# Optimization experiments

Hardware: AMD Instinct MI355X
Metric: run time of the kernel (lower is better)

Reference implementation:

```python
import jax, jax.numpy as jnp
import numpy as np

N_NODES = 100000
N_HE = 50000
N_INC = 600000
D_IN = 256
D_H = 128
N_CLASSES = 40
N_LAYERS = 2


def setup_inputs() -> dict:
    key = jax.random.key(0)
    ks = jax.random.split(key, 8)
    s = lambda d: float(1.0 / np.sqrt(d))
    return {
        "x_0": jax.random.normal(ks[0], (N_NODES, D_IN), jnp.float32),
        "x_1": jax.random.normal(ks[1], (N_HE, D_IN), jnp.float32),
        "node_idx": jax.random.randint(ks[2], (N_INC,), 0, N_NODES),
        "he_idx": jax.random.randint(ks[3], (N_INC,), 0, N_HE),
        "inc_vals": jnp.ones((N_INC,), jnp.float32),
        "W_enc": jax.random.uniform(ks[4], (D_IN, D_H), jnp.float32, -s(D_IN), s(D_IN)),
        "b_enc": jnp.zeros((D_H,), jnp.float32),
        "W_msg0": jax.random.uniform(ks[5], (N_LAYERS, D_H, D_H), jnp.float32, -s(D_H), s(D_H)),
        "b_msg0": jnp.zeros((N_LAYERS, D_H), jnp.float32),
        "W_msg1": jax.random.uniform(ks[6], (N_LAYERS, 2 * D_H, D_H), jnp.float32, -s(2 * D_H), s(2 * D_H)),
        "b_msg1": jnp.zeros((N_LAYERS, D_H), jnp.float32),
        "W_out": jax.random.uniform(ks[7], (D_H, N_CLASSES), jnp.float32, -s(D_H), s(D_H)),
        "b_out": jnp.zeros((N_CLASSES,), jnp.float32),
    }


def reference(x_0, x_1, node_idx, he_idx, inc_vals, W_enc, b_enc,
              W_msg0, b_msg0, W_msg1, b_msg1, W_out, b_out):
    # Encode node/hyperedge features to hidden dim (shared to_hidden_linear).
    x0 = x_0 @ W_enc + b_enc  # (N_NODES, D_H)
    x1 = x_1 @ W_enc + b_enc  # (N_HE, D_H)
    for l in range(N_LAYERS):
        # Node -> hyperedge messaging: m0 = sigmoid(W x0)
        m0 = jax.nn.sigmoid(x0 @ W_msg0[l] + b_msg0[l])  # (N_NODES, D_H)
        # Gather node messages along incidence nnz, weight by incidence values,
        # scatter-sum into hyperedges.
        m0_he = jax.ops.segment_sum(inc_vals[:, None] * m0[node_idx], he_idx,
                                    num_segments=N_HE)  # (N_HE, D_H)
        # Hyperedge -> node messaging: m1 = sigmoid(W [x1 || m0_he])
        m1 = jax.nn.sigmoid(jnp.concatenate([x1, m0_he], axis=-1) @ W_msg1[l] + b_msg1[l])
        m1_node = jax.ops.segment_sum(inc_vals[:, None] * m1[he_idx], node_idx,
                                      num_segments=N_NODES)  # (N_NODES, D_H)
        # Default updating func: sigmoid(x + m) (dropout identity in eval mode).
        x0 = jax.nn.sigmoid(x0 + m1_node)
        x1 = jax.nn.sigmoid(x1 + m0_he)
    return x0 @ W_out + b_out  # (N_NODES, N_CLASSES)
```

## Files before the change

kernel.cpp:

```cpp
#include <hip/hip_runtime.h>
#include <hip/hip_bf16.h>
#include <math.h>

#define N_NODES 100000
#define N_HE    50000
#define N_INC   600000
#define D_IN    256
#define D_H     128
#define N_CLASSES 40

typedef __attribute__((ext_vector_type(8))) short short8;
typedef __attribute__((ext_vector_type(4))) float f32x4;

__device__ __forceinline__ float sigmoidf_(float x) {
    return __builtin_amdgcn_rcpf(1.0f + __expf(-x));
}

__device__ __forceinline__ short bfbits(float f) {
    __hip_bfloat16 h = __float2bfloat16(f);
    return *reinterpret_cast<short*>(&h);
}

__device__ __forceinline__ float bf_lo(unsigned u) { return __uint_as_float(u << 16); }
__device__ __forceinline__ float bf_hi(unsigned u) { return __uint_as_float(u & 0xffff0000u); }
__device__ __forceinline__ unsigned bfpack(float a, float b) {
    return (unsigned)(unsigned short)bfbits(a) | ((unsigned)(unsigned short)bfbits(b) << 16);
}

__device__ __forceinline__ void gload_lds16(const void* g, void* l) {
    __builtin_amdgcn_global_load_lds(
        (const __attribute__((address_space(1))) unsigned int*)g,
        (__attribute__((address_space(3))) unsigned int*)l, 16, 0, 0);
}

__global__ __launch_bounds__(256) void cvt_kernel(
    const float* __restrict__ in, unsigned short* __restrict__ out, int n8)
{
    const int stride = gridDim.x * 256;
    for (int i = blockIdx.x * 256 + threadIdx.x; i < n8; i += stride) {
        const float4 p = *(const float4*)(in + (size_t)i * 8);
        const float4 q = *(const float4*)(in + (size_t)i * 8 + 4);
        uint4 r;
        r.x = bfpack(p.x, p.y); r.y = bfpack(p.z, p.w);
        r.z = bfpack(q.x, q.y); r.w = bfpack(q.z, q.w);
        *(uint4*)(out + (size_t)i * 8) = r;
    }
}

template<int KT, bool SPLIT>
__global__ __launch_bounds__(256) void gemm_st(
    const __hip_bfloat16* __restrict__ A1,
    const __hip_bfloat16* __restrict__ A2,
    const __hip_bfloat16* __restrict__ Wt,
    const float* __restrict__ bias,
    __hip_bfloat16* __restrict__ C,
    int M, int act)
{
    __shared__ uint4 smemv[4096];
    char* const sA = (char*)smemv;
    char* const sB = (char*)smemv + 32768;

    const int tid = threadIdx.x;
    const int wave = tid >> 6, lane = tid & 63;
    const int quad = lane >> 4, nn = lane & 15;
    const int wr = wave >> 1, wc = wave & 1;
    const int row_base = blockIdx.x * 128;
    const int col_base = wc * 64;

    f32x4 acc[4][4] = {};

    for (int h = 0; h < KT; ++h) {
        const char* Asrc = (const char*)(SPLIT ? (h ? A2 : A1) : A1);
        const size_t astride = SPLIT ? 256 : (size_t)KT * 256;
        const size_t aoff = SPLIT ? 0 : (size_t)h * 256;
#pragma unroll
        for (int j = 0; j < 8; ++j) {
            const int sb = j * 4 + wave;
            const int s = sb * 64 + lane;
            const int row = s >> 4, c = s & 15;
            int grow = row_base + row; if (grow >= M) grow = M - 1;
            gload_lds16(Asrc + (size_t)grow * astride + aoff + ((c ^ (row & 7)) * 16),
                        sA + sb * 1024);
        }
#pragma unroll
        for (int j = 0; j < 8; ++j) {
            const int sb = j * 4 + wave;
            const int s = sb * 64 + lane;
            const int n = s >> 4, c = s & 15;
            gload_lds16((const char*)Wt + (size_t)n * (KT * 256) + (size_t)h * 256
                            + ((c ^ (n & 7)) * 16),
                        sB + sb * 1024);
        }
        __syncthreads();

#pragma unroll
        for (int ks = 0; ks < 4; ++ks) {
            short8 a[4], b[4];
#pragma unroll
            for (int rt = 0; rt < 4; ++rt) {
                const int row = wr * 64 + rt * 16 + nn;
                a[rt] = *(const short8*)(sA + row * 256 + (((ks * 4 + quad) ^ (row & 7)) * 16));
            }
#pragma unroll
            for (int ct = 0; ct < 4; ++ct) {
                const int n = col_base + ct * 16 + nn;
                b[ct] = *(const short8*)(sB + n * 256 + (((ks * 4 + quad) ^ (n & 7)) * 16));
            }
#pragma unroll
            for (int ct = 0; ct < 4; ++ct)
#pragma unroll
                for (int rt = 0; rt < 4; ++rt)
                    acc[rt][ct] = __builtin_amdgcn_mfma_f32_16x16x32_bf16(
                        a[rt], b[ct], acc[rt][ct], 0, 0, 0);
        }
        __syncthreads();
    }

    float bs[4];
#pragma unroll
    for (int ct = 0; ct < 4; ++ct) bs[ct] = bias[col_base + ct * 16 + nn];

    constexpr int KP = 136;
    unsigned short* sC = (unsigned short*)smemv;
#pragma unroll
    for (int rt = 0; rt < 4; ++rt) {
#pragma unroll
        for (int i = 0; i < 4; ++i) {
            const int R = wr * 64 + rt * 16 + quad * 4 + i;
#pragma unroll
            for (int ct = 0; ct < 4; ++ct) {
                float v = acc[rt][ct][i] + bs[ct];
                if (act) v = sigmoidf_(v);
                sC[R * KP + col_base + ct * 16 + nn] = (unsigned short)bfbits(v);
            }
        }
    }
    __syncthreads();

    {
        const int row = tid >> 1, half = tid & 1;
        const int gr = row_base + row;
        if (gr < M) {
            const unsigned short* srcp = sC + row * KP + half * 64;
            uint4* dstp = (uint4*)(C + (size_t)gr * 128 + half * 64);
#pragma unroll
            for (int j = 0; j < 8; ++j) dstp[j] = *(const uint4*)(srcp + j * 8);
        }
    }
}

__global__ __launch_bounds__(256) void out_gemm_mfma(
    const __hip_bfloat16* __restrict__ X,
    const __hip_bfloat16* __restrict__ Wt,
    const float* __restrict__ b, float* __restrict__ out, int M)
{
    constexpr int KP = 136;
    __shared__ uint4 sXv[1024];
    __shared__ __hip_bfloat16 sW[48 * KP];
    __shared__ float sB[48];
    __shared__ float sO[64 * 44];

    char* const sX = (char*)sXv;
    const int tid = threadIdx.x;
    const int wave = tid >> 6, lane = tid & 63;

#pragma unroll
    for (int j = 0; j < 4; ++j) {
        const int sb = j * 4 + wave;
        const int s = sb * 64 + lane;
        const int row = s >> 4, c = s & 15;
        int grow = blockIdx.x * 64 + row; if (grow >= M) grow = M - 1;
        gload_lds16((const char*)X + (size_t)grow * 256 + ((c ^ (row & 7)) * 16),
                    sX + sb * 1024);
    }
    for (int c = tid; c < 48 * 16; c += 256) {
        const int n = c >> 4, ko = (c & 15) * 8;
        *(uint4*)&sW[n * KP + ko] = *(const uint4*)&Wt[n * 128 + ko];
    }
    if (tid < 48) sB[tid] = (tid < 40) ? b[tid] : 0.0f;
    __syncthreads();

    const int quad = lane >> 4, nn = lane & 15;

    f32x4 acc[3] = {};
#pragma unroll
    for (int ks = 0; ks < 4; ++ks) {
        const int rowl = wave * 16 + nn;
        const short8 a = *(const short8*)(sX + rowl * 256 + (((ks * 4 + quad) ^ (rowl & 7)) * 16));
#pragma unroll
        for (int ct = 0; ct < 3; ++ct) {
            const short8 bf = *(const short8*)&sW[(ct * 16 + nn) * KP + ks * 32 + quad * 8];
            acc[ct] = __builtin_amdgcn_mfma_f32_16x16x32_bf16(a, bf, acc[ct], 0, 0, 0);
        }
    }

#pragma unroll
    for (int ct = 0; ct < 3; ++ct) {
        const int c = ct * 16 + nn;
        if (c < 40) {
#pragma unroll
            for (int i = 0; i < 4; ++i) {
                const int rl = wave * 16 + quad * 4 + i;
                sO[rl * 44 + c] = acc[ct][i] + sB[c];
            }
        }
    }
    __syncthreads();

    for (int c = tid; c < 640; c += 256) {
        const int row = c / 10, ch = c % 10;
        const int gr = blockIdx.x * 64 + row;
        if (gr < M)
            *(float4*)(out + (size_t)gr * 40 + ch * 4) =
                *(const float4*)(sO + row * 44 + ch * 4);
    }
}

__global__ __launch_bounds__(256) void wprep_kernel(
    const float* __restrict__ We, const float* __restrict__ Wm0,
    const float* __restrict__ Wm1, const float* __restrict__ Wout,
    __hip_bfloat16* __restrict__ Wt_enc, __hip_bfloat16* __restrict__ Wt_m0,
    __hip_bfloat16* __restrict__ Wt_m1, __hip_bfloat16* __restrict__ Wt_out)
{
    const int i = blockIdx.x * 256 + threadIdx.x;
    if (i < 32768) {
        const int n = i >> 8, k = i & 255;
        Wt_enc[n * 256 + k] = __float2bfloat16(We[k * 128 + n]);
    } else if (i < 65536) {
        int j = i - 32768; const int l = j >> 14; j &= 16383;
        const int n = j >> 7, k = j & 127;
        Wt_m0[l * 16384 + n * 128 + k] = __float2bfloat16(Wm0[l * 16384 + k * 128 + n]);
    } else if (i < 131072) {
        int j = i - 65536; const int l = j >> 15; j &= 32767;
        const int n = j >> 8, k = j & 255;
        Wt_m1[l * 32768 + n * 256 + k] = __float2bfloat16(Wm1[l * 32768 + k * 128 + n]);
    } else {
        const int j = i - 131072;
        const int n = j >> 7, k = j & 127;
        Wt_out[n * 128 + k] = (n < 40) ? __float2bfloat16(Wout[k * 40 + n])
                                       : __float2bfloat16(0.0f);
    }
}

__global__ __launch_bounds__(256) void zero_int_kernel(int* __restrict__ p, int n)
{
    const int i = blockIdx.x * 256 + threadIdx.x;
    if (i < n) p[i] = 0;
}

__global__ __launch_bounds__(256) void hist_kernel(
    const int* __restrict__ he_idx, const int* __restrict__ node_idx,
    int* __restrict__ he_cnt, int* __restrict__ node_cnt,
    int* __restrict__ he_rank, int* __restrict__ node_rank, int n)
{
    const int i = blockIdx.x * 256 + threadIdx.x;
    if (i < n) {
        he_rank[i] = atomicAdd(&he_cnt[he_idx[i]], 1);
        node_rank[i] = atomicAdd(&node_cnt[node_idx[i]], 1);
    }
}

__global__ __launch_bounds__(256) void scan1_kernel(
    int* __restrict__ data, int* __restrict__ bsums, int n)
{
    __shared__ int s[256];
    const int t = threadIdx.x;
    const int base = blockIdx.x * 1024 + t * 4;
    int4 v = make_int4(0, 0, 0, 0);
    if (base < n) v = *(const int4*)(data + base);
    s[t] = v.x + v.y + v.z + v.w;
    __syncthreads();
    for (int d = 1; d < 256; d <<= 1) {
        const int u = (t >= d) ? s[t - d] : 0;
        __syncthreads();
        s[t] += u;
        __syncthreads();
    }
    if (t == 255) bsums[blockIdx.x] = s[255];
    int e = t ? s[t - 1] : 0;
    if (base < n) {
        int4 o;
        o.x = e; e += v.x; o.y = e; e += v.y; o.z = e; e += v.z; o.w = e;
        *(int4*)(data + base) = o;
    }
}

__global__ __launch_bounds__(256) void scan2_kernel(int* __restrict__ bsums, int nb)
{
    __shared__ int s[256];
    const int t = threadIdx.x;
    const int v = (t < nb) ? bsums[t] : 0;
    s[t] = v;
    __syncthreads();
    for (int d = 1; d < 256; d <<= 1) {
        const int u = (t >= d) ? s[t - d] : 0;
        __syncthreads();
        s[t] += u;
        __syncthreads();
    }
    if (t < nb) bsums[t] = s[t] - v;
}

__global__ __launch_bounds__(256) void scan3_kernel(
    int* __restrict__ data, const int* __restrict__ bsums, int n)
{
    const int base = blockIdx.x * 1024 + threadIdx.x * 4;
    if (base >= n) return;
    const int adj = bsums[blockIdx.x] - ((base >= N_HE) ? N_INC : 0);
    int4 v = *(int4*)(data + base);
    v.x += adj; v.y += adj; v.z += adj; v.w += adj;
    *(int4*)(data + base) = v;
}

__global__ __launch_bounds__(256) void fill_kernel(
    const int* __restrict__ node_idx, const int* __restrict__ he_idx,
    const float* __restrict__ vals,
    const int* __restrict__ he_off, const int* __restrict__ node_off,
    const int* __restrict__ he_rank, const int* __restrict__ node_rank,
    int2* __restrict__ he_edge, int2* __restrict__ node_edge, int n)
{
    const int e = blockIdx.x * 256 + threadIdx.x;
    if (e >= n) return;
    const int hn = he_idx[e], nd = node_idx[e];
    const int vb = __float_as_int(vals[e]);
    he_edge[he_off[hn] + he_rank[e]] = make_int2(nd, vb);
    node_edge[node_off[nd] + node_rank[e]] = make_int2(hn, vb);
}

__device__ __forceinline__ void reduce_groups(
    int lane, float a0, float a1, float a2, float a3,
    float a4, float a5, float a6, float a7, float& s0, float& s1)
{
    const bool hb = (lane & 32) != 0;
    float t0 = hb ? a0 : a4;
    float t1 = hb ? a1 : a5;
    float t2 = hb ? a2 : a6;
    float t3 = hb ? a3 : a7;
    float r0 = __shfl_xor(t0, 32);
    float r1 = __shfl_xor(t1, 32);
    float r2 = __shfl_xor(t2, 32);
    float r3 = __shfl_xor(t3, 32);
    float e0 = (hb ? a4 : a0) + r0;
    float e1 = (hb ? a5 : a1) + r1;
    float e2 = (hb ? a6 : a2) + r2;
    float e3 = (hb ? a7 : a3) + r3;
    const bool lb = (lane & 16) != 0;
    float u0 = lb ? e0 : e2;
    float u1 = lb ? e1 : e3;
    float q0 = __shfl_xor(u0, 16);
    float q1 = __shfl_xor(u1, 16);
    s0 = (lb ? e2 : e0) + q0;
    s1 = (lb ? e3 : e1) + q1;
}

__global__ __launch_bounds__(256) void gather_he_kernel(
    const __hip_bfloat16* __restrict__ msrc,
    const __hip_bfloat16* __restrict__ x1cur,
    __hip_bfloat16* __restrict__ m0_he,
    __hip_bfloat16* __restrict__ x1next,
    const int* __restrict__ off, const int2* __restrict__ edges, int n_seg)
{
    const int wave = threadIdx.x >> 6;
    const int lane = threadIdx.x & 63;
    const int row = blockIdx.x * 4 + wave;
    if (row >= n_seg) return;
    const int start = off[row];
    const int end = (row + 1 < n_seg) ? off[row + 1] : N_INC;
    const int g = lane >> 4;
    const int l16 = lane & 15;
    float a0 = 0.f, a1 = 0.f, a2 = 0.f, a3 = 0.f;
    float a4 = 0.f, a5 = 0.f, a6 = 0.f, a7 = 0.f;
    const unsigned short* s16 = (const unsigned short*)msrc;
    int e = start;
    for (; e + 4 <= end; e += 4) {
        const int2 ed = edges[e + g];
        const float v = __int_as_float(ed.y);
        const uint4 u = *(const uint4*)(s16 + (size_t)ed.x * 128 + l16 * 8);
        a0 += bf_lo(u.x) * v; a1 += bf_hi(u.x) * v;
        a2 += bf_lo(u.y) * v; a3 += bf_hi(u.y) * v;
        a4 += bf_lo(u.z) * v; a5 += bf_hi(u.z) * v;
        a6 += bf_lo(u.w) * v; a7 += bf_hi(u.w) * v;
    }
    if (e < end) {
        const int ee = e + g;
        const int2 ed = (ee < end) ? edges[ee] : make_int2(0, 0);
        const float v = __int_as_float(ed.y);
        const uint4 u = *(const uint4*)(s16 + (size_t)ed.x * 128 + l16 * 8);
        a0 += bf_lo(u.x) * v; a1 += bf_hi(u.x) * v;
        a2 += bf_lo(u.y) * v; a3 += bf_hi(u.y) * v;
        a4 += bf_lo(u.z) * v; a5 += bf_hi(u.z) * v;
        a6 += bf_lo(u.w) * v; a7 += bf_hi(u.w) * v;
    }
    float s0, s1;
    reduce_groups(lane, a0, a1, a2, a3, a4, a5, a6, a7, s0, s1);
    const size_t o32 = (size_t)row * 64 + l16 * 4 + g;
    ((unsigned*)m0_he)[o32] = bfpack(s0, s1);
    const unsigned xu = ((const unsigned*)x1cur)[o32];
    ((unsigned*)x1next)[o32] =
        bfpack(sigmoidf_(bf_lo(xu) + s0), sigmoidf_(bf_hi(xu) + s1));
}

__global__ __launch_bounds__(256) void gather_node_kernel(
    const __hip_bfloat16* __restrict__ msrc,
    __hip_bfloat16* __restrict__ x0,
    const int* __restrict__ off, const int2* __restrict__ edges, int n_seg)
{
    const int wave = threadIdx.x >> 6;
    const int lane = threadIdx.x & 63;
    const int row = blockIdx.x * 4 + wave;
    if (row >= n_seg) return;
    const int start = off[row];
    const int end = (row + 1 < n_seg) ? off[row + 1] : N_INC;
    const int g = lane >> 4;
    const int l16 = lane & 15;
    float a0 = 0.f, a1 = 0.f, a2 = 0.f, a3 = 0.f;
    float a4 = 0.f, a5 = 0.f, a6 = 0.f, a7 = 0.f;
    const unsigned short* s16 = (const unsigned short*)msrc;
    int e = start;
    for (; e + 4 <= end; e += 4) {
        const int2 ed = edges[e + g];
        const float v = __int_as_float(ed.y);
        const uint4 u = *(const uint4*)(s16 + (size_t)ed.x * 128 + l16 * 8);
        a0 += bf_lo(u.x) * v; a1 += bf_hi(u.x) * v;
        a2 += bf_lo(u.y) * v; a3 += bf_hi(u.y) * v;
        a4 += bf_lo(u.z) * v; a5 += bf_hi(u.z) * v;
        a6 += bf_lo(u.w) * v; a7 += bf_hi(u.w) * v;
    }
    if (e < end) {
        const int ee = e + g;
        const int2 ed = (ee < end) ? edges[ee] : make_int2(0, 0);
        const float v = __int_as_float(ed.y);
        const uint4 u = *(const uint4*)(s16 + (size_t)ed.x * 128 + l16 * 8);
        a0 += bf_lo(u.x) * v; a1 += bf_hi(u.x) * v;
        a2 += bf_lo(u.y) * v; a3 += bf_hi(u.y) * v;
        a4 += bf_lo(u.z) * v; a5 += bf_hi(u.z) * v;
        a6 += bf_lo(u.w) * v; a7 += bf_hi(u.w) * v;
    }
    float s0, s1;
    reduce_groups(lane, a0, a1, a2, a3, a4, a5, a6, a7, s0, s1);
    const size_t o32 = (size_t)row * 64 + l16 * 4 + g;
    unsigned* px = (unsigned*)x0 + o32;
    const unsigned xu = *px;
    *px = bfpack(sigmoidf_(bf_lo(xu) + s0), sigmoidf_(bf_hi(xu) + s1));
}

extern "C" void kernel_launch(void* const* d_in, const int* in_sizes, int n_in,
                              void* d_out, int out_size, void* d_ws, size_t ws_size,
                              hipStream_t stream)
{
    const float* x0_in   = (const float*)d_in[0];
    const float* x1_in   = (const float*)d_in[1];
    const int*   node_idx = (const int*)d_in[2];
    const int*   he_idx   = (const int*)d_in[3];
    const float* inc_vals = (const float*)d_in[4];
    const float* W_enc   = (const float*)d_in[5];
    const float* b_enc   = (const float*)d_in[6];
    const float* W_msg0  = (const float*)d_in[7];
    const float* b_msg0  = (const float*)d_in[8];
    const float* W_msg1  = (const float*)d_in[9];
    const float* b_msg1  = (const float*)d_in[10];
    const float* W_out   = (const float*)d_in[11];
    const float* b_out   = (const float*)d_in[12];
    float* out = (float*)d_out;

    __hip_bfloat16* x0h    = (__hip_bfloat16*)d_ws;
    __hip_bfloat16* x1a    = x0h + 12800000;
    __hip_bfloat16* x1b    = x1a + 6400000;
    __hip_bfloat16* mbuf   = x1b + 6400000;
    __hip_bfloat16* m0_he  = mbuf + 12800000;
    __hip_bfloat16* Wt_enc = m0_he + 6400000;
    __hip_bfloat16* Wt_m0  = Wt_enc + 32768;
    __hip_bfloat16* Wt_m1  = Wt_m0 + 32768;
    __hip_bfloat16* Wt_out = Wt_m1 + 65536;
    int*  he_off    = (int*)(Wt_out + 6144);
    int*  node_off  = he_off + N_HE;
    int*  bsums     = node_off + N_NODES;
    int*  he_rank   = bsums + 256;
    int*  node_rank = he_rank + N_INC;
    int2* he_edge   = (int2*)(node_rank + N_INC);
    int2* node_edge = he_edge + N_INC;

    __hip_bfloat16* x0bf = x1b;
    __hip_bfloat16* x1bf = x1b;

    zero_int_kernel<<<(N_HE + N_NODES + 255) / 256, 256, 0, stream>>>(
        he_off, N_HE + N_NODES);
    hist_kernel<<<(N_INC + 255) / 256, 256, 0, stream>>>(
        he_idx, node_idx, he_off, node_off, he_rank, node_rank, N_INC);
    const int scan_n = N_HE + N_NODES;
    const int scan_blocks = (scan_n + 1023) / 1024;
    scan1_kernel<<<scan_blocks, 256, 0, stream>>>(he_off, bsums, scan_n);
    scan2_kernel<<<1, 256, 0, stream>>>(bsums, scan_blocks);
    scan3_kernel<<<scan_blocks, 256, 0, stream>>>(he_off, bsums, scan_n);
    fill_kernel<<<(N_INC + 255) / 256, 256, 0, stream>>>(
        node_idx, he_idx, inc_vals, he_off, node_off, he_rank, node_rank,
        he_edge, node_edge, N_INC);

    wprep_kernel<<<536, 256, 0, stream>>>(W_enc, W_msg0, W_msg1, W_out,
                                          Wt_enc, Wt_m0, Wt_m1, Wt_out);

    cvt_kernel<<<2048, 256, 0, stream>>>(x0_in, (unsigned short*)x0bf, 3200000);
    gemm_st<2, false><<<(N_NODES + 127) / 128, 256, 0, stream>>>(
        x0bf, nullptr, Wt_enc, b_enc, x0h, N_NODES, 0);
    cvt_kernel<<<2048, 256, 0, stream>>>(x1_in, (unsigned short*)x1bf, 1600000);
    gemm_st<2, false><<<(N_HE + 127) / 128, 256, 0, stream>>>(
        x1bf, nullptr, Wt_enc, b_enc, x1a, N_HE, 0);

    __hip_bfloat16* x1cur = x1a;
    __hip_bfloat16* x1nxt = x1b;
    for (int l = 0; l < 2; ++l) {
        gemm_st<1, false><<<(N_NODES + 127) / 128, 256, 0, stream>>>(
            x0h, nullptr, Wt_m0 + (size_t)l * 16384,
            b_msg0 + (size_t)l * 128, mbuf, N_NODES, 1);
        gather_he_kernel<<<(N_HE + 3) / 4, 256, 0, stream>>>(
            mbuf, x1cur, m0_he, x1nxt, he_off, he_edge, N_HE);
        gemm_st<2, true><<<(N_HE + 127) / 128, 256, 0, stream>>>(
            x1cur, m0_he, Wt_m1 + (size_t)l * 32768,
            b_msg1 + (size_t)l * 128, mbuf, N_HE, 1);
        gather_node_kernel<<<(N_NODES + 3) / 4, 256, 0, stream>>>(
            mbuf, x0h, node_off, node_edge, N_NODES);
        __hip_bfloat16* t = x1cur; x1cur = x1nxt; x1nxt = t;
    }

    out_gemm_mfma<<<(N_NODES + 63) / 64, 256, 0, stream>>>(
        x0h, Wt_out, b_out, out, N_NODES);
}
```

Before: 572.4 us.

## Fuse fp32-to-bf16 conversion into encoder GEMM and merge small setup kernels

The encoder GEMM now reads fp32 inputs directly, converts them to bf16 in registers and stores them into swizzled LDS. This removes the separate conversion kernels and the intermediate bf16 buffer round-trip. The counter zeroing is folded into the weight-prep kernel, and the two final scan passes are merged, with each block recomputing its prefix from the block sums. The A operand loads now go through registers rather than async global-to-LDS copies, which may reduce load/compute overlap.

```diff
diff --git a/kernel.cpp b/kernel.cpp
--- a/kernel.cpp
+++ b/kernel.cpp
@@ -31,20 +31,6 @@
     __builtin_amdgcn_global_load_lds(
         (const __attribute__((address_space(1))) unsigned int*)g,
         (__attribute__((address_space(3))) unsigned int*)l, 16, 0, 0);
-}
-
-__global__ __launch_bounds__(256) void cvt_kernel(
-    const float* __restrict__ in, unsigned short* __restrict__ out, int n8)
-{
-    const int stride = gridDim.x * 256;
-    for (int i = blockIdx.x * 256 + threadIdx.x; i < n8; i += stride) {
-        const float4 p = *(const float4*)(in + (size_t)i * 8);
-        const float4 q = *(const float4*)(in + (size_t)i * 8 + 4);
-        uint4 r;
-        r.x = bfpack(p.x, p.y); r.y = bfpack(p.z, p.w);
-        r.z = bfpack(q.x, q.y); r.w = bfpack(q.z, q.w);
-        *(uint4*)(out + (size_t)i * 8) = r;
-    }
 }
 
 template<int KT, bool SPLIT>
@@ -149,6 +135,106 @@
     }
 }
 
+__global__ __launch_bounds__(256) void gemm_enc(
+    const float* __restrict__ A,
+    const __hip_bfloat16* __restrict__ Wt,
+    const float* __restrict__ bias,
+    __hip_bfloat16* __restrict__ C,
+    int M)
+{
+    __shared__ uint4 smemv[4096];
+    char* const sA = (char*)smemv;
+    char* const sB = (char*)smemv + 32768;
+
+    const int tid = threadIdx.x;
+    const int wave = tid >> 6, lane = tid & 63;
+    const int quad = lane >> 4, nn = lane & 15;
+    const int wr = wave >> 1, wc = wave & 1;
+    const int row_base = blockIdx.x * 128;
+    const int col_base = wc * 64;
+
+    f32x4 acc[4][4] = {};
+
+    for (int h = 0; h < 2; ++h) {
+#pragma unroll
+        for (int j = 0; j < 8; ++j) {
+            const int sb = j * 4 + wave;
+            const int s = sb * 64 + lane;
+            const int n = s >> 4, c = s & 15;
+            gload_lds16((const char*)Wt + (size_t)n * 512 + (size_t)h * 256
+                            + ((c ^ (n & 7)) * 16),
+                        sB + sb * 1024);
+        }
+#pragma unroll
+        for (int j = 0; j < 8; ++j) {
+            const int s = j * 256 + tid;
+            const int row = s >> 4, c = s & 15;
+            int grow = row_base + row; if (grow >= M) grow = M - 1;
+            const float* ap = A + (size_t)grow * 256 + h * 128 + c * 8;
+            const float4 p = *(const float4*)ap;
+            const float4 q = *(const float4*)(ap + 4);
+            uint4 r;
+            r.x = bfpack(p.x, p.y); r.y = bfpack(p.z, p.w);
+            r.z = bfpack(q.x, q.y); r.w = bfpack(q.z, q.w);
+            *(uint4*)(sA + row * 256 + ((c ^ (row & 7)) * 16)) = r;
+        }
+        __syncthreads();
+
+#pragma unroll
+        for (int ks = 0; ks < 4; ++ks) {
+            short8 a[4], b[4];
+#pragma unroll
+            for (int rt = 0; rt < 4; ++rt) {
+                const int row = wr * 64 + rt * 16 + nn;
+                a[rt] = *(const short8*)(sA + row * 256 + (((ks * 4 + quad) ^ (row & 7)) * 16));
+            }
+#pragma unroll
+            for (int ct = 0; ct < 4; ++ct) {
+                const int n = col_base + ct * 16 + nn;
+                b[ct] = *(const short8*)(sB + n * 256 + (((ks * 4 + quad) ^ (n & 7)) * 16));
+            }
+#pragma unroll
+            for (int ct = 0; ct < 4; ++ct)
+#pragma unroll
+                for (int rt = 0; rt < 4; ++rt)
+                    acc[rt][ct] = __builtin_amdgcn_mfma_f32_16x16x32_bf16(
+                        a[rt], b[ct], acc[rt][ct], 0, 0, 0);
+        }
+        __syncthreads();
+    }
+
+    float bs[4];
+#pragma unroll
+    for (int ct = 0; ct < 4; ++ct) bs[ct] = bias[col_base + ct * 16 + nn];
+
+    constexpr int KP = 136;
+    unsigned short* sC = (unsigned short*)smemv;
+#pragma unroll
+    for (int rt = 0; rt < 4; ++rt) {
+#pragma unroll
+        for (int i = 0; i < 4; ++i) {
+            const int R = wr * 64 + rt * 16 + quad * 4 + i;
+#pragma unroll
+            for (int ct = 0; ct < 4; ++ct) {
+                const float v = acc[rt][ct][i] + bs[ct];
+                sC[R * KP + col_base + ct * 16 + nn] = (unsigned short)bfbits(v);
+            }
+        }
+    }
+    __syncthreads();
+
+    {
+        const int row = tid >> 1, half = tid & 1;
+        const int gr = row_base + row;
+        if (gr < M) {
+            const unsigned short* srcp = sC + row * KP + half * 64;
+            uint4* dstp = (uint4*)(C + (size_t)gr * 128 + half * 64);
+#pragma unroll
+            for (int j = 0; j < 8; ++j) dstp[j] = *(const uint4*)(srcp + j * 8);
+        }
+    }
+}
+
 __global__ __launch_bounds__(256) void out_gemm_mfma(
     const __hip_bfloat16* __restrict__ X,
     const __hip_bfloat16* __restrict__ Wt,
@@ -216,11 +302,12 @@
     }
 }
 
-__global__ __launch_bounds__(256) void wprep_kernel(
+__global__ __launch_bounds__(256) void prep_kernel(
     const float* __restrict__ We, const float* __restrict__ Wm0,
     const float* __restrict__ Wm1, const float* __restrict__ Wout,
     __hip_bfloat16* __restrict__ Wt_enc, __hip_bfloat16* __restrict__ Wt_m0,
-    __hip_bfloat16* __restrict__ Wt_m1, __hip_bfloat16* __restrict__ Wt_out)
+    __hip_bfloat16* __restrict__ Wt_m1, __hip_bfloat16* __restrict__ Wt_out,
+    int* __restrict__ cnt_zero)
 {
     const int i = blockIdx.x * 256 + threadIdx.x;
     if (i < 32768) {
@@ -234,18 +321,15 @@
         int j = i - 65536; const int l = j >> 15; j &= 32767;
         const int n = j >> 8, k = j & 255;
         Wt_m1[l * 32768 + n * 256 + k] = __float2bfloat16(Wm1[l * 32768 + k * 128 + n]);
-    } else {
+    } else if (i < 137216) {
         const int j = i - 131072;
         const int n = j >> 7, k = j & 127;
         Wt_out[n * 128 + k] = (n < 40) ? __float2bfloat16(Wout[k * 40 + n])
                                        : __float2bfloat16(0.0f);
-    }
-}
-
-__global__ __launch_bounds__(256) void zero_int_kernel(int* __restrict__ p, int n)
-{
-    const int i = blockIdx.x * 256 + threadIdx.x;
-    if (i < n) p[i] = 0;
+    } else {
+        const int z = i - 137216;
+        if (z < N_HE + N_NODES) cnt_zero[z] = 0;
+    }
 }
 
 __global__ __launch_bounds__(256) void hist_kernel(
@@ -285,11 +369,12 @@
     }
 }
 
-__global__ __launch_bounds__(256) void scan2_kernel(int* __restrict__ bsums, int nb)
+__global__ __launch_bounds__(256) void scan23_kernel(
+    int* __restrict__ data, const int* __restrict__ bsums, int n, int nb)
 {
     __shared__ int s[256];
     const int t = threadIdx.x;
-    const int v = (t < nb) ? bsums[t] : 0;
+    const int v = (t < nb && t < (int)blockIdx.x) ? bsums[t] : 0;
     s[t] = v;
     __syncthreads();
     for (int d = 1; d < 256; d <<= 1) {
@@ -298,18 +383,13 @@
         s[t] += u;
         __syncthreads();
     }
-    if (t < nb) bsums[t] = s[t] - v;
-}
-
-__global__ __launch_bounds__(256) void scan3_kernel(
-    int* __restrict__ data, const int* __restrict__ bsums, int n)
-{
-    const int base = blockIdx.x * 1024 + threadIdx.x * 4;
+    const int total = s[255];
+    const int base = blockIdx.x * 1024 + t * 4;
     if (base >= n) return;
-    const int adj = bsums[blockIdx.x] - ((base >= N_HE) ? N_INC : 0);
-    int4 v = *(int4*)(data + base);
-    v.x += adj; v.y += adj; v.z += adj; v.w += adj;
-    *(int4*)(data + base) = v;
+    const int adj = total - ((base >= N_HE) ? N_INC : 0);
+    int4 vv = *(int4*)(data + base);
+    vv.x += adj; vv.y += adj; vv.z += adj; vv.w += adj;
+    *(int4*)(data + base) = vv;
 }
 
 __global__ __launch_bounds__(256) void fill_kernel(
@@ -480,31 +560,23 @@
     int2* he_edge   = (int2*)(node_rank + N_INC);
     int2* node_edge = he_edge + N_INC;
 
-    __hip_bfloat16* x0bf = x1b;
-    __hip_bfloat16* x1bf = x1b;
-
-    zero_int_kernel<<<(N_HE + N_NODES + 255) / 256, 256, 0, stream>>>(
-        he_off, N_HE + N_NODES);
+    prep_kernel<<<(137216 + N_HE + N_NODES + 255) / 256, 256, 0, stream>>>(
+        W_enc, W_msg0, W_msg1, W_out, Wt_enc, Wt_m0, Wt_m1, Wt_out, he_off);
+
     hist_kernel<<<(N_INC + 255) / 256, 256, 0, stream>>>(
         he_idx, node_idx, he_off, node_off, he_rank, node_rank, N_INC);
     const int scan_n = N_HE + N_NODES;
     const int scan_blocks = (scan_n + 1023) / 1024;
     scan1_kernel<<<scan_blocks, 256, 0, stream>>>(he_off, bsums, scan_n);
-    scan2_kernel<<<1, 256, 0, stream>>>(bsums, scan_blocks);
-    scan3_kernel<<<scan_blocks, 256, 0, stream>>>(he_off, bsums, scan_n);
+    scan23_kernel<<<scan_blocks, 256, 0, stream>>>(he_off, bsums, scan_n, scan_blocks);
     fill_kernel<<<(N_INC + 255) / 256, 256, 0, stream>>>(
         node_idx, he_idx, inc_vals, he_off, node_off, he_rank, node_rank,
         he_edge, node_edge, N_INC);
 
-    wprep_kernel<<<536, 256, 0, stream>>>(W_enc, W_msg0, W_msg1, W_out,
-                                          Wt_enc, Wt_m0, Wt_m1, Wt_out);
-
-    cvt_kernel<<<2048, 256, 0, stream>>>(x0_in, (unsigned short*)x0bf, 3200000);
-    gemm_st<2, false><<<(N_NODES + 127) / 128, 256, 0, stream>>>(
-        x0bf, nullptr, Wt_enc, b_enc, x0h, N_NODES, 0);
-    cvt_kernel<<<2048, 256, 0, stream>>>(x1_in, (unsigned short*)x1bf, 1600000);
-    gemm_st<2, false><<<(N_HE + 127) / 128, 256, 0, stream>>>(
-        x1bf, nullptr, Wt_enc, b_enc, x1a, N_HE, 0);
+    gemm_enc<<<(N_NODES + 127) / 128, 256, 0, stream>>>(
+        x0_in, Wt_enc, b_enc, x0h, N_NODES);
+    gemm_enc<<<(N_HE + 127) / 128, 256, 0, stream>>>(
+        x1_in, Wt_enc, b_enc, x1a, N_HE);
 
     __hip_bfloat16* x1cur = x1a;
     __hip_bfloat16* x1nxt = x1b;
```

Measured after the change: 547.3 us. 1.05x faster.
